# Kernel optimization log

Measured on AMD Instinct MI355X. Metric: run time of the kernel, lower is better.

## Reference

```python
import jax, jax.numpy as jnp
import numpy as np


def setup_inputs() -> dict:
    key = jax.random.key(0)
    k1, k2, k3 = jax.random.split(key, 3)
    L, B, H = 256, 8, 512
    inputs = jax.random.normal(k1, (L, B, H), dtype=jnp.float32)
    attn_W = jax.random.normal(k2, (H, 2 * H), dtype=jnp.float32) * 0.02
    attn_b = jnp.zeros((H,), dtype=jnp.float32)
    score_W = jax.random.normal(k3, (1, H), dtype=jnp.float32) * 0.02
    score_b = jnp.zeros((1,), dtype=jnp.float32)
    return {"inputs": inputs, "attn_W": attn_W, "attn_b": attn_b,
            "score_W": score_W, "score_b": score_b}


def reference(inputs, attn_W, attn_b, score_W, score_b):
    # inputs: [L, B, H]; attn_W: [H, 2H] (torch Linear weight), attn_b: [H]
    # score_W: [1, H], score_b: [1]
    H = attn_W.shape[0]
    # Decompose Linear(cat(sen1, sen2)) = sen1 @ W1^T + sen2 @ W2^T + b
    W1 = attn_W[:, :H]   # [H, H] acts on sen1 (row index i)
    W2 = attn_W[:, H:]   # [H, H] acts on sen2 (col index j)
    x = jnp.transpose(inputs, (1, 0, 2))          # [B, L, H]
    p1 = jnp.einsum('blh,oh->blo', x, W1)         # [B, L, H]
    p2 = jnp.einsum('blh,oh->blo', x, W2)         # [B, L, H]
    # feat[b,i,j,:] = tanh(attn(cat(x[b,i], x[b,j])))  -> [B, L, L, H]
    feat = jnp.tanh(p1[:, :, None, :] + p2[:, None, :, :] + attn_b)
    # score Linear H -> 1, squeeze last dim -> [B, L, L]
    energies = jnp.einsum('bijh,h->bij', feat, score_W[0]) + score_b[0]
    # softmax over dim=1 (the sen1 / i axis), as in the torch code
    return jax.nn.softmax(energies, axis=1)
```

## Files before the change

### kernel.cpp

```cpp
#include <hip/hip_runtime.h>

#define LOG2E 1.4426950408889634f
#define SCALE (2.0f * LOG2E)

__device__ __forceinline__ float fast_exp2(float x) { return __builtin_amdgcn_exp2f(x); }
__device__ __forceinline__ float fast_rcp(float x)  { return __builtin_amdgcn_rcpf(x); }

typedef __attribute__((ext_vector_type(8))) short bf16x8;
typedef __attribute__((ext_vector_type(4))) float f32x4;

__global__ __launch_bounds__(256) void pack_kernel(const float* __restrict__ inputs,
                                                   const float* __restrict__ attn_W,
                                                   ushort* __restrict__ Ap,
                                                   ushort* __restrict__ Bp) {
    __shared__ ushort Hs[64 * 136];
    __shared__ ushort Ls[64 * 136];

    const int bid = blockIdx.x;
    const bool isA = bid < 128;
    const int sub = isA ? bid : bid - 128;
    const int tb = sub >> 2;
    const int kc = sub & 3;
    const int t = threadIdx.x;

#pragma unroll
    for (int it = 0; it < 4; ++it) {
        const int u = it * 256 + t;
        const int row = u >> 4;
        const int kc8 = u & 15;
        const float* src;
        if (isA) {
            int sr = ((tb & 3) * 64 + row) * 8 + (tb >> 2);
            src = inputs + (long)sr * 512 + kc * 128 + kc8 * 8;
        } else {
            int r = (tb & 7) * 64 + row;
            src = attn_W + (long)r * 1024 + (tb >> 3) * 512 + kc * 128 + kc8 * 8;
        }
        float4 v0 = *(const float4*)src;
        float4 v1 = *(const float4*)(src + 4);
        float vv[8] = {v0.x, v0.y, v0.z, v0.w, v1.x, v1.y, v1.z, v1.w};
        ushort hi8[8], lo8[8];
#pragma unroll
        for (int j = 0; j < 8; ++j) {
            unsigned u32 = __float_as_uint(vv[j]);
            unsigned h = (u32 + 0x7FFF + ((u32 >> 16) & 1)) >> 16;
            hi8[j] = (ushort)h;
            float lo = vv[j] - __uint_as_float(h << 16);
            unsigned ul = __float_as_uint(lo);
            lo8[j] = (ushort)((ul + 0x7FFF + ((ul >> 16) & 1)) >> 16);
        }
        const int lidx = row * 136 + kc8 * 8;
        *(uint4*)&Hs[lidx] = *(const uint4*)hi8;
        *(uint4*)&Ls[lidx] = *(const uint4*)lo8;
    }
    __syncthreads();

    ushort* P = (isA ? Ap : Bp) + (long)tb * 98304;
#pragma unroll
    for (int it = 0; it < 4; ++it) {
        const int u = it * 256 + t;
        const int l  = u & 63;
        const int fr = (u >> 6) & 3;
        const int ks = (u >> 8) & 1;
        const int ktl = (u >> 9) & 1;
        const int j = fr * 16 + (l & 15);
        const int klocal = ktl * 64 + ks * 32 + (l >> 4) * 8;
        uint4 h  = *(const uint4*)&Hs[j * 136 + klocal];
        uint4 lo = *(const uint4*)&Ls[j * 136 + klocal];
        const int kt0 = kc * 2 + ktl;
        const long off = (long)ks * 2048 + fr * 512 + l * 8;
        if (isA) {
            *(uint4*)(P + (kt0 +  0) * 4096 + off) = h;
            *(uint4*)(P + (kt0 + 16) * 4096 + off) = h;
            *(uint4*)(P + (kt0 +  8) * 4096 + off) = lo;
        } else {
            *(uint4*)(P + (kt0 +  0) * 4096 + off) = h;
            *(uint4*)(P + (kt0 +  8) * 4096 + off) = h;
            *(uint4*)(P + (kt0 + 16) * 4096 + off) = lo;
        }
    }
}

__global__ __launch_bounds__(512) void mfma_gemm(const ushort* __restrict__ Ap,
                                                 const ushort* __restrict__ Bp,
                                                 const float* __restrict__ attn_b,
                                                 float* __restrict__ E1,
                                                 float* __restrict__ E2) {
    const int xcd = blockIdx.x & 7;
    const int idx = blockIdx.x >> 3;
    const int mb  = xcd * 2 + (idx >> 4);
    const int nb  = idx & 15;
    __shared__ ushort lds[2][12288];

    const int t = threadIdx.x;
    const int lane = t & 63, w = t >> 6;
    const int wr = w >> 1, wc = w & 1;

    const ushort* A0 = Ap + (long)(mb * 2 + 0) * 98304;
    const ushort* A1 = Ap + (long)(mb * 2 + 1) * 98304;
    const ushort* B0 = Bp + (long)nb * 98304;

    f32x4 acc[2][2];
#pragma unroll
    for (int i = 0; i < 2; ++i)
#pragma unroll
        for (int j = 0; j < 2; ++j)
            acc[i][j] = (f32x4){0.f, 0.f, 0.f, 0.f};

    uint4 st[3];
#define LOADK(kt)                                                  \
    {                                                              \
        st[0] = ((const uint4*)(A0 + (kt) * 4096))[t];             \
        st[1] = ((const uint4*)(A1 + (kt) * 4096))[t];             \
        st[2] = ((const uint4*)(B0 + (kt) * 4096))[t];             \
    }
#define STOREK(bf)                                                 \
    {                                                              \
        uint4* d = (uint4*)lds[bf];                                \
        d[t] = st[0]; d[t + 512] = st[1]; d[t + 1024] = st[2];     \
    }

    LOADK(0);
    STOREK(0);
    __syncthreads();

    for (int kt = 0; kt < 24; ++kt) {
        if (kt < 23) LOADK(kt + 1);
        const ushort* buf = lds[kt & 1];
#pragma unroll
        for (int ks = 0; ks < 2; ++ks) {
            bf16x8 a[2], b[2];
            const int abase = (wr >> 1) * 4096 + ks * 2048 + (wr & 1) * 1024 + lane * 8;
            const int bbase = 8192 + ks * 2048 + wc * 1024 + lane * 8;
            a[0] = *(const bf16x8*)&buf[abase];
            a[1] = *(const bf16x8*)&buf[abase + 512];
            b[0] = *(const bf16x8*)&buf[bbase];
            b[1] = *(const bf16x8*)&buf[bbase + 512];
#pragma unroll
            for (int mf = 0; mf < 2; ++mf)
#pragma unroll
                for (int nf = 0; nf < 2; ++nf)
                    acc[mf][nf] = __builtin_amdgcn_mfma_f32_16x16x32_bf16(
                        a[mf], b[nf], acc[mf][nf], 0, 0, 0);
        }
        if (kt < 23) {
            STOREK((kt + 1) & 1);
            __syncthreads();
        }
    }
#undef LOADK
#undef STOREK

#pragma unroll
    for (int nf = 0; nf < 2; ++nf) {
        int n = nb * 64 + wc * 32 + nf * 16 + (lane & 15);
        const bool isE1 = (n < 512);
        float* dst = isE1 ? E1 : E2;
        int o = n & 511;
        float bias = isE1 ? attn_b[o] : 0.0f;
#pragma unroll
        for (int mf = 0; mf < 2; ++mf) {
            int ml = mb * 128 + wr * 32 + mf * 16 + ((lane >> 4) << 2);
            int bb = ml >> 8, l = ml & 255;
            long rowoff = ((long)(bb * 8 + (l >> 5)) * 512 + o) * 32 + (l & 31);
#pragma unroll
            for (int r = 0; r < 4; ++r)
                dst[rowoff + r] = fast_exp2(SCALE * (acc[mf][nf][r] + bias));
        }
    }
}

__global__ __launch_bounds__(256) void energy_kernel(const float* __restrict__ E1,
                                                     const float* __restrict__ E2,
                                                     const float* __restrict__ sW,
                                                     float* __restrict__ EP) {
    const int bid = blockIdx.x;
    const int s  = bid & 3;
    const int tj = (bid >> 2) & 7;
    const int ti = (bid >> 5) & 7;
    const int b  = bid >> 8;
    __shared__ float p1s[64 * 32];
    __shared__ float p2s[64 * 32];
    __shared__ float csh[128];

    const int t = threadIdx.x;
    const int tx = t & 15, ty = t >> 4;

    if (t < 128) csh[t] = 2.0f * sW[s * 128 + t];

    const float* p1base = E1 + ((long)(b * 8 + ti) * 512 + s * 128) * 32;
    const float* p2base = E2 + ((long)(b * 8 + tj) * 512 + s * 128) * 32;

    float acc00 = 0.f, acc01 = 0.f, acc10 = 0.f, acc11 = 0.f;

    for (int c0 = 0; c0 < 128; c0 += 64) {
        __syncthreads();
        const float4* s1 = (const float4*)(p1base + c0 * 32);
        const float4* s2 = (const float4*)(p2base + c0 * 32);
        float4* d1 = (float4*)p1s;
        float4* d2 = (float4*)p2s;
        d1[t] = s1[t];  d1[256 + t] = s1[256 + t];
        d2[t] = s2[t];  d2[256 + t] = s2[256 + t];
        __syncthreads();
#pragma unroll 8
        for (int hh = 0; hh < 64; ++hh) {
            float c = csh[c0 + hh];
            float2 a  = *(const float2*)&p1s[hh * 32 + ty * 2];
            float2 bj = *(const float2*)&p2s[hh * 32 + tx * 2];
            acc00 = fmaf(c, fast_rcp(fmaf(a.x, bj.x, 1.0f)), acc00);
            acc01 = fmaf(c, fast_rcp(fmaf(a.x, bj.y, 1.0f)), acc01);
            acc10 = fmaf(c, fast_rcp(fmaf(a.y, bj.x, 1.0f)), acc10);
            acc11 = fmaf(c, fast_rcp(fmaf(a.y, bj.y, 1.0f)), acc11);
        }
    }

    float* Eb = EP + (long)s * 524288 + (long)b * 65536 + (ti * 32) * 256 + tj * 32;
    *(float2*)&Eb[(ty * 2 + 0) * 256 + tx * 2] = make_float2(acc00, acc01);
    *(float2*)&Eb[(ty * 2 + 1) * 256 + tx * 2] = make_float2(acc10, acc11);
}

__global__ __launch_bounds__(256) void softmax_kernel(const float* __restrict__ P0,
                                                      const float* __restrict__ P1,
                                                      const float* __restrict__ P2,
                                                      const float* __restrict__ P3,
                                                      float* __restrict__ out) {
    const int b  = blockIdx.x >> 4;
    const int jt = blockIdx.x & 15;
    const int t  = threadIdx.x;
    const int jx = t & 15;
    const int iy = t >> 4;
    const long base = (long)b * 65536 + jt * 16 + jx;

    float v[16];
#pragma unroll
    for (int k = 0; k < 16; ++k) {
        long idx = base + (long)(iy + k * 16) * 256;
        v[k] = -(P0[idx] + P1[idx] + P2[idx] + P3[idx]);
    }

    float m = v[0];
#pragma unroll
    for (int k = 1; k < 16; ++k) m = fmaxf(m, v[k]);

    __shared__ float red[256];
    red[t] = m;
    __syncthreads();
    if (t < 128) red[t] = fmaxf(red[t], red[t + 128]);
    __syncthreads();
    if (t < 64) red[t] = fmaxf(red[t], red[t + 64]);
    __syncthreads();
    if (t < 32) red[t] = fmaxf(red[t], red[t + 32]);
    __syncthreads();
    if (t < 16) red[t] = fmaxf(red[t], red[t + 16]);
    __syncthreads();
    m = red[jx];
    __syncthreads();

    float ssum = 0.f;
#pragma unroll
    for (int k = 0; k < 16; ++k) {
        v[k] = fast_exp2((v[k] - m) * LOG2E);
        ssum += v[k];
    }
    red[t] = ssum;
    __syncthreads();
    if (t < 128) red[t] += red[t + 128];
    __syncthreads();
    if (t < 64) red[t] += red[t + 64];
    __syncthreads();
    if (t < 32) red[t] += red[t + 32];
    __syncthreads();
    if (t < 16) red[t] += red[t + 16];
    __syncthreads();
    float inv = fast_rcp(red[jx]);

#pragma unroll
    for (int k = 0; k < 16; ++k) {
        long idx = base + (long)(iy + k * 16) * 256;
        out[idx] = v[k] * inv;
    }
}

extern "C" void kernel_launch(void* const* d_in, const int* in_sizes, int n_in,
                              void* d_out, int out_size, void* d_ws, size_t ws_size,
                              hipStream_t stream) {
    const float* inputs  = (const float*)d_in[0];
    const float* attn_W  = (const float*)d_in[1];
    const float* attn_b  = (const float*)d_in[2];
    const float* score_W = (const float*)d_in[3];
    float* out = (float*)d_out;

    float* ws = (float*)d_ws;
    float* E1 = ws;
    float* E2 = ws + (1 << 20);
    float* EP = ws + (2 << 20);
    ushort* Ap = (ushort*)(ws + (4 << 20));
    ushort* Bp = Ap + 3145728;

    pack_kernel<<<192, 256, 0, stream>>>(inputs, attn_W, Ap, Bp);
    mfma_gemm<<<256, 512, 0, stream>>>(Ap, Bp, attn_b, E1, E2);
    energy_kernel<<<2048, 256, 0, stream>>>(E1, E2, score_W, EP);
    softmax_kernel<<<128, 256, 0, stream>>>(EP, EP + 524288, EP + 2 * 524288,
                                            EP + 3 * 524288, out);
}
```

Before: 62.88 us.

## Pair h-terms to share one reciprocal and enlarge energy tile per thread

The energy kernel now merges two consecutive hidden-dimension terms c0/ya + c1/yb into (c0*yb + c1*ya)/(ya*yb), halving the number of transcendental reciprocal instructions. Each thread also computes a 4x2 output tile instead of 2x2, with a 64x32 block tile, which halves the grid and improves LDS reuse per load. The cost is a few extra multiplies, higher register use, and a possible loss of precision or overflow in the product of two denominators.

```diff
diff --git a/kernel.cpp b/kernel.cpp
--- a/kernel.cpp
+++ b/kernel.cpp
@@ -177,10 +177,10 @@
     const int bid = blockIdx.x;
     const int s  = bid & 3;
     const int tj = (bid >> 2) & 7;
-    const int ti = (bid >> 5) & 7;
-    const int b  = bid >> 8;
-    __shared__ float p1s[64 * 32];
-    __shared__ float p2s[64 * 32];
+    const int ti = (bid >> 5) & 3;
+    const int b  = bid >> 7;
+    __shared__ float As[64 * 64];
+    __shared__ float Bs[64 * 32];
     __shared__ float csh[128];
 
     const int t = threadIdx.x;
@@ -188,35 +188,69 @@
 
     if (t < 128) csh[t] = 2.0f * sW[s * 128 + t];
 
-    const float* p1base = E1 + ((long)(b * 8 + ti) * 512 + s * 128) * 32;
-    const float* p2base = E2 + ((long)(b * 8 + tj) * 512 + s * 128) * 32;
-
-    float acc00 = 0.f, acc01 = 0.f, acc10 = 0.f, acc11 = 0.f;
+    const float* e1base = E1 + ((long)(b * 8 + ti * 2) * 512 + s * 128) * 32;
+    const float* e2base = E2 + ((long)(b * 8 + tj) * 512 + s * 128) * 32;
+
+    float acc[4][2];
+#pragma unroll
+    for (int i = 0; i < 4; ++i) { acc[i][0] = 0.f; acc[i][1] = 0.f; }
 
     for (int c0 = 0; c0 < 128; c0 += 64) {
         __syncthreads();
-        const float4* s1 = (const float4*)(p1base + c0 * 32);
-        const float4* s2 = (const float4*)(p2base + c0 * 32);
-        float4* d1 = (float4*)p1s;
-        float4* d2 = (float4*)p2s;
-        d1[t] = s1[t];  d1[256 + t] = s1[256 + t];
-        d2[t] = s2[t];  d2[256 + t] = s2[256 + t];
+        {
+            const float4* s1 = (const float4*)(e1base + (long)c0 * 32);
+#pragma unroll
+            for (int it = 0; it < 4; ++it) {
+                int f = it * 256 + t;
+                int ol = f >> 4;
+                int i4 = (f & 15) * 4;
+                int half = i4 >> 5, ii = i4 & 31;
+                float4 v = s1[(half * 16384 + ol * 32 + ii) >> 2];
+                *(float4*)&As[ol * 64 + i4] = v;
+            }
+            const float4* s2 = (const float4*)(e2base + (long)c0 * 32);
+#pragma unroll
+            for (int it = 0; it < 2; ++it) {
+                int f = it * 256 + t;
+                int ol = f >> 3;
+                int j4 = (f & 7) * 4;
+                float4 v = s2[(ol * 32 + j4) >> 2];
+                *(float4*)&Bs[ol * 32 + j4] = v;
+            }
+        }
         __syncthreads();
-#pragma unroll 8
-        for (int hh = 0; hh < 64; ++hh) {
-            float c = csh[c0 + hh];
-            float2 a  = *(const float2*)&p1s[hh * 32 + ty * 2];
-            float2 bj = *(const float2*)&p2s[hh * 32 + tx * 2];
-            acc00 = fmaf(c, fast_rcp(fmaf(a.x, bj.x, 1.0f)), acc00);
-            acc01 = fmaf(c, fast_rcp(fmaf(a.x, bj.y, 1.0f)), acc01);
-            acc10 = fmaf(c, fast_rcp(fmaf(a.y, bj.x, 1.0f)), acc10);
-            acc11 = fmaf(c, fast_rcp(fmaf(a.y, bj.y, 1.0f)), acc11);
-        }
-    }
-
-    float* Eb = EP + (long)s * 524288 + (long)b * 65536 + (ti * 32) * 256 + tj * 32;
-    *(float2*)&Eb[(ty * 2 + 0) * 256 + tx * 2] = make_float2(acc00, acc01);
-    *(float2*)&Eb[(ty * 2 + 1) * 256 + tx * 2] = make_float2(acc10, acc11);
+
+#pragma unroll 4
+        for (int p = 0; p < 32; ++p) {
+            const float c0v = csh[c0 + 2 * p];
+            const float c1v = csh[c0 + 2 * p + 1];
+            float4 a0 = *(const float4*)&As[(2 * p) * 64 + ty * 4];
+            float4 a1 = *(const float4*)&As[(2 * p + 1) * 64 + ty * 4];
+            float2 b0 = *(const float2*)&Bs[(2 * p) * 32 + tx * 2];
+            float2 b1 = *(const float2*)&Bs[(2 * p + 1) * 32 + tx * 2];
+            const float a0v[4] = {a0.x, a0.y, a0.z, a0.w};
+            const float a1v[4] = {a1.x, a1.y, a1.z, a1.w};
+            const float b0v[2] = {b0.x, b0.y};
+            const float b1v[2] = {b1.x, b1.y};
+#pragma unroll
+            for (int i = 0; i < 4; ++i) {
+#pragma unroll
+                for (int j = 0; j < 2; ++j) {
+                    float ya = fmaf(a0v[i], b0v[j], 1.0f);
+                    float yb = fmaf(a1v[i], b1v[j], 1.0f);
+                    float num = fmaf(c0v, yb, c1v * ya);
+                    float den = ya * yb;
+                    acc[i][j] = fmaf(num, fast_rcp(den), acc[i][j]);
+                }
+            }
+        }
+    }
+
+    float* Eb = EP + (long)s * 524288 + (long)b * 65536 +
+                (long)(ti * 64 + ty * 4) * 256 + tj * 32 + tx * 2;
+#pragma unroll
+    for (int i = 0; i < 4; ++i)
+        *(float2*)&Eb[i * 256] = make_float2(acc[i][0], acc[i][1]);
 }
 
 __global__ __launch_bounds__(256) void softmax_kernel(const float* __restrict__ P0,
@@ -299,7 +333,7 @@
 
     pack_kernel<<<192, 256, 0, stream>>>(inputs, attn_W, Ap, Bp);
     mfma_gemm<<<256, 512, 0, stream>>>(Ap, Bp, attn_b, E1, E2);
-    energy_kernel<<<2048, 256, 0, stream>>>(E1, E2, score_W, EP);
+    energy_kernel<<<1024, 256, 0, stream>>>(E1, E2, score_W, EP);
     softmax_kernel<<<128, 256, 0, stream>>>(EP, EP + 524288, EP + 2 * 524288,
                                             EP + 3 * 524288, out);
 }
```

Measured after the change: 58.73 us. -6.6%, faster.

## Combine four reciprocals into one and enlarge energy tile to 64x64

Applied to the files above, without the earlier changes.

The energy kernel now computes a 64x64 (i,j) tile per block with a 4x4 register micro-tile per thread, in place of 32x32 with 2x2. This raises shared-memory reuse and cuts the grid from 2048 blocks to 512. It also sums four c/y terms over a common denominator, so each group of four h values needs one hardware reciprocal instead of four. The cost is more multiplies, more register pressure, and a possible loss of precision or overflow in the product of four y values.

```diff
diff --git a/kernel.cpp b/kernel.cpp
--- a/kernel.cpp
+++ b/kernel.cpp
@@ -175,12 +175,12 @@
                                                      const float* __restrict__ sW,
                                                      float* __restrict__ EP) {
     const int bid = blockIdx.x;
-    const int s  = bid & 3;
-    const int tj = (bid >> 2) & 7;
-    const int ti = (bid >> 5) & 7;
-    const int b  = bid >> 8;
-    __shared__ float p1s[64 * 32];
-    __shared__ float p2s[64 * 32];
+    const int tj = bid & 3;
+    const int ti = (bid >> 2) & 3;
+    const int b  = (bid >> 4) & 7;
+    const int s  = bid >> 7;
+    __shared__ float As[32 * 64];
+    __shared__ float Bs[32 * 64];
     __shared__ float csh[128];
 
     const int t = threadIdx.x;
@@ -188,35 +188,71 @@
 
     if (t < 128) csh[t] = 2.0f * sW[s * 128 + t];
 
-    const float* p1base = E1 + ((long)(b * 8 + ti) * 512 + s * 128) * 32;
-    const float* p2base = E2 + ((long)(b * 8 + tj) * 512 + s * 128) * 32;
-
-    float acc00 = 0.f, acc01 = 0.f, acc10 = 0.f, acc11 = 0.f;
-
-    for (int c0 = 0; c0 < 128; c0 += 64) {
+    const float* e1base = E1 + (long)(b * 8 + ti * 2) * 16384;
+    const float* e2base = E2 + (long)(b * 8 + tj * 2) * 16384;
+
+    float acc[4][4];
+#pragma unroll
+    for (int i = 0; i < 4; ++i)
+#pragma unroll
+        for (int j = 0; j < 4; ++j) acc[i][j] = 0.f;
+
+    for (int c0 = 0; c0 < 128; c0 += 32) {
         __syncthreads();
-        const float4* s1 = (const float4*)(p1base + c0 * 32);
-        const float4* s2 = (const float4*)(p2base + c0 * 32);
-        float4* d1 = (float4*)p1s;
-        float4* d2 = (float4*)p2s;
-        d1[t] = s1[t];  d1[256 + t] = s1[256 + t];
-        d2[t] = s2[t];  d2[256 + t] = s2[256 + t];
+#pragma unroll
+        for (int it = 0; it < 2; ++it) {
+            const int f = it * 256 + t;
+            const int ol = f >> 4;
+            const int i4 = (f & 15) * 4;
+            const long srcoff = (long)(i4 >> 5) * 16384 + (long)(s * 128 + c0 + ol) * 32 + (i4 & 31);
+            *(float4*)&As[ol * 64 + i4] = *(const float4*)(e1base + srcoff);
+            *(float4*)&Bs[ol * 64 + i4] = *(const float4*)(e2base + srcoff);
+        }
         __syncthreads();
-#pragma unroll 8
-        for (int hh = 0; hh < 64; ++hh) {
-            float c = csh[c0 + hh];
-            float2 a  = *(const float2*)&p1s[hh * 32 + ty * 2];
-            float2 bj = *(const float2*)&p2s[hh * 32 + tx * 2];
-            acc00 = fmaf(c, fast_rcp(fmaf(a.x, bj.x, 1.0f)), acc00);
-            acc01 = fmaf(c, fast_rcp(fmaf(a.x, bj.y, 1.0f)), acc01);
-            acc10 = fmaf(c, fast_rcp(fmaf(a.y, bj.x, 1.0f)), acc10);
-            acc11 = fmaf(c, fast_rcp(fmaf(a.y, bj.y, 1.0f)), acc11);
-        }
-    }
-
-    float* Eb = EP + (long)s * 524288 + (long)b * 65536 + (ti * 32) * 256 + tj * 32;
-    *(float2*)&Eb[(ty * 2 + 0) * 256 + tx * 2] = make_float2(acc00, acc01);
-    *(float2*)&Eb[(ty * 2 + 1) * 256 + tx * 2] = make_float2(acc10, acc11);
+
+#pragma unroll 2
+        for (int p = 0; p < 8; ++p) {
+            const float4 c4 = *(const float4*)&csh[c0 + p * 4];
+            float4 a0 = *(const float4*)&As[(p * 4 + 0) * 64 + ty * 4];
+            float4 a1 = *(const float4*)&As[(p * 4 + 1) * 64 + ty * 4];
+            float4 a2 = *(const float4*)&As[(p * 4 + 2) * 64 + ty * 4];
+            float4 a3 = *(const float4*)&As[(p * 4 + 3) * 64 + ty * 4];
+            float4 b0 = *(const float4*)&Bs[(p * 4 + 0) * 64 + tx * 4];
+            float4 b1 = *(const float4*)&Bs[(p * 4 + 1) * 64 + tx * 4];
+            float4 b2 = *(const float4*)&Bs[(p * 4 + 2) * 64 + tx * 4];
+            float4 b3 = *(const float4*)&Bs[(p * 4 + 3) * 64 + tx * 4];
+            const float a0v[4] = {a0.x, a0.y, a0.z, a0.w};
+            const float a1v[4] = {a1.x, a1.y, a1.z, a1.w};
+            const float a2v[4] = {a2.x, a2.y, a2.z, a2.w};
+            const float a3v[4] = {a3.x, a3.y, a3.z, a3.w};
+            const float b0v[4] = {b0.x, b0.y, b0.z, b0.w};
+            const float b1v[4] = {b1.x, b1.y, b1.z, b1.w};
+            const float b2v[4] = {b2.x, b2.y, b2.z, b2.w};
+            const float b3v[4] = {b3.x, b3.y, b3.z, b3.w};
+#pragma unroll
+            for (int i = 0; i < 4; ++i) {
+#pragma unroll
+                for (int j = 0; j < 4; ++j) {
+                    float y0 = fmaf(a0v[i], b0v[j], 1.0f);
+                    float y1 = fmaf(a1v[i], b1v[j], 1.0f);
+                    float y2 = fmaf(a2v[i], b2v[j], 1.0f);
+                    float y3 = fmaf(a3v[i], b3v[j], 1.0f);
+                    float y01 = y0 * y1, y23 = y2 * y3;
+                    float d = y01 * y23;
+                    float n01 = fmaf(c4.x, y1, c4.y * y0);
+                    float n23 = fmaf(c4.z, y3, c4.w * y2);
+                    float n = fmaf(n01, y23, n23 * y01);
+                    acc[i][j] = fmaf(n, fast_rcp(d), acc[i][j]);
+                }
+            }
+        }
+    }
+
+    float* Eb = EP + (long)s * 524288 + (long)b * 65536 +
+                (long)(ti * 64 + ty * 4) * 256 + tj * 64 + tx * 4;
+#pragma unroll
+    for (int i = 0; i < 4; ++i)
+        *(float4*)&Eb[i * 256] = make_float4(acc[i][0], acc[i][1], acc[i][2], acc[i][3]);
 }
 
 __global__ __launch_bounds__(256) void softmax_kernel(const float* __restrict__ P0,
@@ -299,7 +335,7 @@
 
     pack_kernel<<<192, 256, 0, stream>>>(inputs, attn_W, Ap, Bp);
     mfma_gemm<<<256, 512, 0, stream>>>(Ap, Bp, attn_b, E1, E2);
-    energy_kernel<<<2048, 256, 0, stream>>>(E1, E2, score_W, EP);
+    energy_kernel<<<512, 256, 0, stream>>>(E1, E2, score_W, EP);
     softmax_kernel<<<128, 256, 0, stream>>>(EP, EP + 524288, EP + 2 * 524288,
                                             EP + 3 * 524288, out);
 }
```

Result: faster. 57.40 us (-8.7%).
